# Optimization experiments

Measured on AMD Instinct MI355X. Metric: run time of the kernel, lower is better.

## Reference

```python
import jax, jax.numpy as jnp
import numpy as np

B, N, E, F, C = 4, 10000, 160000, 128, 128
NUM_ITERATIONS = 3  # num_iterations init arg


def setup_inputs() -> dict:
    key = jax.random.key(0)
    ks = jax.random.split(key, 8)
    objects = jax.random.normal(ks[0], (B, N, F), dtype=jnp.float32)
    connections = jax.random.randint(ks[1], (B, E, 2), 0, N, dtype=jnp.int32)
    # small init scales keep exp() in the attention numerically tame (mirrors
    # glorot/orthogonal-scale weights at init)
    object_state_W = jax.random.normal(ks[2], (F, C), dtype=jnp.float32) * (1.0 / np.sqrt(F))
    state_attention_W = jax.random.normal(ks[3], (C, C), dtype=jnp.float32) * 0.05
    linked_state_attention_W = jax.random.normal(ks[4], (C, C), dtype=jnp.float32) * 0.05
    linked_state_W = jax.random.normal(ks[5], (C, C), dtype=jnp.float32) * (1.0 / np.sqrt(C))
    attention_b = jnp.zeros((C,), dtype=jnp.float32)
    state_b = jnp.zeros((C,), dtype=jnp.float32)
    return {
        "objects": objects,
        "object_state_W": object_state_W,
        "state_attention_W": state_attention_W,
        "linked_state_attention_W": linked_state_attention_W,
        "attention_b": attention_b,
        "linked_state_W": linked_state_W,
        "state_b": state_b,
        "connections": connections,
    }


def reference(objects, object_state_W, state_attention_W, linked_state_attention_W,
              attention_b, linked_state_W, state_b, connections):
    # bidirectional: double edges with both orientations  [B, 2E]
    src = jnp.concatenate([connections[:, :, 0], connections[:, :, 1]], axis=1)
    dst = jnp.concatenate([connections[:, :, 1], connections[:, :, 0]], axis=1)

    # initial states: [B, N, C]
    states = jnp.tanh(jnp.einsum('bnf,fc->bnc', objects, object_state_W) + state_b)

    def step_one(states_b, src_b, dst_b):
        # states_b: [N, C]; src_b/dst_b: [2E]
        states_aW = states_b @ state_attention_W          # [N, C]
        linked_aW = states_b @ linked_state_attention_W   # [N, C]
        # per-edge unnormalized attention  [2E, C]
        attention = jnp.exp(states_aW[src_b] + linked_aW[dst_b] + attention_b)
        # scatter-add normalization; self edge contributes 1 (exp(0))
        attention_norm = jnp.ones_like(states_b).at[src_b].add(attention)  # [N, C]
        self_attention = 1.0 / attention_norm
        attention = attention / attention_norm[src_b]
        # weighted neighbor aggregation
        attented = attention * states_b[dst_b]                              # [2E, C]
        linked_gated = jnp.zeros_like(states_b).at[src_b].add(attented)     # [N, C]
        return jnp.tanh(states_b * self_attention + linked_gated @ linked_state_W + state_b)

    step = jax.vmap(step_one)
    for _ in range(NUM_ITERATIONS):
        states = step(states, src, dst)
    return states
```

## Files before the change

### kernel.cpp

```cpp
#include <hip/hip_runtime.h>
#include <hip/hip_bf16.h>


#define BATCH 4
#define NNODE 10000
#define NEDGE 160000
#define TWOE  (2*NEDGE)
#define MROWS (BATCH*NNODE)
#define NCHUNK 64
#define CHUNKE (NEDGE/NCHUNK)
#define PADN  10240
#define EDPAD (TWOE + 8*NNODE)

typedef unsigned short u16;
typedef unsigned int   u32;
typedef __attribute__((ext_vector_type(8))) short bf16x8_t;
typedef __attribute__((ext_vector_type(4))) float f32x4_t;

__device__ __forceinline__ float b2f(u16 h){ return __uint_as_float(((u32)h) << 16); }
__device__ __forceinline__ u16 f2bf(float f){
  u32 u = __float_as_uint(f);
  return (u16)((u + 0x7fffu + ((u >> 16) & 1u)) >> 16);
}
__device__ __forceinline__ float fast_tanh(float x){
  float e = __expf(2.0f * x);
  return fmaf(-2.0f, __builtin_amdgcn_rcpf(e + 1.0f), 1.0f);
}

__device__ __forceinline__ void chunk_of(int blk, int& b, int& c){
  int xcd = blk & 7;
  b = xcd >> 1;
  c = ((blk >> 3) << 1) | (xcd & 1);
}

__global__ void __launch_bounds__(256) k1_prep_hist(const int* __restrict__ conn,
    u16* __restrict__ partial,
    const void* __restrict__ objects,
    const void* __restrict__ Wo, const void* __restrict__ Wa,
    const void* __restrict__ Wla, const void* __restrict__ Wl,
    const void* __restrict__ ab, const void* __restrict__ sb,
    int* __restrict__ flag, u16* __restrict__ Wt, float* __restrict__ biasf){
  __shared__ u32 hist[NNODE / 2];
  __shared__ int zc, hc;
  if (blockIdx.x < 256){
    int b, c; chunk_of(blockIdx.x, b, c);
    for (int n = threadIdx.x; n < NNODE / 2; n += 256) hist[n] = 0;
    __syncthreads();
    const int2* cp = (const int2*)conn + (size_t)b * NEDGE + c * CHUNKE;
    for (int i = threadIdx.x; i < CHUNKE; i += 256){
      int2 e = cp[i];
      atomicAdd(&hist[e.x >> 1], 1u << ((e.x & 1) << 4));
      atomicAdd(&hist[e.y >> 1], 1u << ((e.y & 1) << 4));
    }
    __syncthreads();
    u16* prow = partial + (size_t)(b * NCHUNK + c) * PADN;
    for (int n = threadIdx.x; n < NNODE; n += 256)
      prow[n] = (u16)(hist[n >> 1] >> ((n & 1) << 4));
  } else {
    if (threadIdx.x == 0){ zc = 0; hc = 0; }
    __syncthreads();
    const u32* objw = (const u32*)objects;
    int z = 0, hcnt = 0;
    for (int i = threadIdx.x; i < 1024; i += 256){
      u32 lo = objw[i] & 0xffffu;
      if (lo == 0) z++;
      if (((lo >> 7) & 0xffu) >= 160u) hcnt++;
    }
    atomicAdd(&zc, z); atomicAdd(&hc, hcnt);
    __syncthreads();
    bool f = (hc > 0 || zc > 512);
    int p = blockIdx.x - 256;
    if (p == 0 && threadIdx.x == 0) *flag = f ? 1 : 0;
    int idx = p * 256 + threadIdx.x;
    if (idx < 65536){
      int m = idx >> 14, k = (idx >> 7) & 127, c = idx & 127;
      const void* src = (m == 0) ? Wo : (m == 1) ? Wa : (m == 2) ? Wla : Wl;
      u16 h = f ? f2bf(((const float*)src)[k * 128 + c]) : ((const u16*)src)[k * 128 + c];
      Wt[m * 16384 + c * 128 + k] = h;
    } else {
      int t = idx - 65536;
      const void* src = (t < 128) ? sb : ab;
      int i = t & 127;
      biasf[t] = f ? ((const float*)src)[i] : b2f(((const u16*)src)[i]);
    }
  }
}

__global__ void __launch_bounds__(256) csr_colscan(u16* __restrict__ partial,
    int* __restrict__ row_start, int* __restrict__ bsum, int* __restrict__ deg){
  int b = blockIdx.x / 40, w = blockIdx.x % 40;
  int n = w * 256 + threadIdx.x;
  u32 run = 0;
  if (n < NNODE){
    #pragma unroll 8
    for (int c = 0; c < NCHUNK; c++){
      size_t idx = (size_t)(b * NCHUNK + c) * PADN + n;
      u32 v = partial[idx];
      partial[idx] = (u16)run;
      run += v;
    }
  }
  u32 pad = (run + 7u) & ~7u;
  __shared__ u32 buf[256];
  buf[threadIdx.x] = pad;
  __syncthreads();
  for (int off = 1; off < 256; off <<= 1){
    u32 x = (threadIdx.x >= (unsigned)off) ? buf[threadIdx.x - off] : 0;
    __syncthreads();
    buf[threadIdx.x] += x;
    __syncthreads();
  }
  u32 incl = buf[threadIdx.x];
  if (n < NNODE){
    row_start[b * (NNODE + 1) + n] = (int)(incl - pad);
    deg[b * NNODE + n] = (int)run;
  }
  if (threadIdx.x == 255) bsum[blockIdx.x] = (int)incl;
}

__global__ void scanC(int* __restrict__ row_start, const int* __restrict__ bsum){
  int b = blockIdx.x / 40, j = blockIdx.x % 40;
  int n = j * 256 + threadIdx.x;
  int off = 0;
  for (int q = b * 40; q < b * 40 + j; q++) off += bsum[q];
  if (n < NNODE) row_start[b * (NNODE + 1) + n] += off;
  if (j == 39 && threadIdx.x == 0)
    row_start[b * (NNODE + 1) + NNODE] = off + bsum[b * 40 + 39];
}

__device__ __forceinline__ void gemm_tile4(const u16* __restrict__ arow,
    const u16* __restrict__ wt, int lm, int lq, int cofs, f32x4_t acc[4]){
  #pragma unroll
  for (int ks = 0; ks < 4; ks++){
    bf16x8_t a = *(const bf16x8_t*)(arow + ks * 32);
    #pragma unroll
    for (int nb = 0; nb < 4; nb++){
      bf16x8_t bfr = *(const bf16x8_t*)(wt + (cofs + nb * 16 + lm) * 128 + ks * 32 + lq * 8);
      acc[nb] = __builtin_amdgcn_mfma_f32_16x16x32_bf16(a, bfr, acc[nb], 0, 0, 0);
    }
  }
}

__device__ __forceinline__ void gemm_tile4_packed(const u32* __restrict__ Lrow,
    const u16* __restrict__ wt, int lm, int lq, int cofs, f32x4_t acc[4]){
  #pragma unroll
  for (int ks = 0; ks < 4; ks++){
    uint4 wa = *(const uint4*)(Lrow + ks * 32 + lq * 8);
    uint4 wb = *(const uint4*)(Lrow + ks * 32 + lq * 8 + 4);
    bf16x8_t a;
    a[0] = (short)wa.x; a[1] = (short)wa.y; a[2] = (short)wa.z; a[3] = (short)wa.w;
    a[4] = (short)wb.x; a[5] = (short)wb.y; a[6] = (short)wb.z; a[7] = (short)wb.w;
    #pragma unroll
    for (int nb = 0; nb < 4; nb++){
      bf16x8_t bfr = *(const bf16x8_t*)(wt + (cofs + nb * 16 + lm) * 128 + ks * 32 + lq * 8);
      acc[nb] = __builtin_amdgcn_mfma_f32_16x16x32_bf16(a, bfr, acc[nb], 0, 0, 0);
    }
  }
}

__device__ __forceinline__ void phase2_awlaw4(const u16* __restrict__ ldstile,
    const u16* __restrict__ Wt, const float* __restrict__ biasf,
    int lm, int lq, int cofs, int r0, _Float16* __restrict__ eat,
    u32* __restrict__ ghw){
  const u16* Wta  = Wt + 16384;
  const u16* Wtla = Wt + 32768;
  const u16* ldsrow = ldstile + lm * 136 + lq * 8;
  f32x4_t accA[4], accL[4];
  #pragma unroll
  for (int i = 0; i < 4; i++){ accA[i] = (f32x4_t){0.f,0.f,0.f,0.f}; accL[i] = (f32x4_t){0.f,0.f,0.f,0.f}; }
  #pragma unroll
  for (int ks = 0; ks < 4; ks++){
    bf16x8_t a = *(const bf16x8_t*)(ldsrow + ks * 32);
    #pragma unroll
    for (int nb = 0; nb < 4; nb++){
      bf16x8_t ba = *(const bf16x8_t*)(Wta  + (cofs + nb * 16 + lm) * 128 + ks * 32 + lq * 8);
      bf16x8_t bl = *(const bf16x8_t*)(Wtla + (cofs + nb * 16 + lm) * 128 + ks * 32 + lq * 8);
      accA[nb] = __builtin_amdgcn_mfma_f32_16x16x32_bf16(a, ba, accA[nb], 0, 0, 0);
      accL[nb] = __builtin_amdgcn_mfma_f32_16x16x32_bf16(a, bl, accL[nb], 0, 0, 0);
    }
  }
  #pragma unroll
  for (int nb = 0; nb < 4; nb++){
    int col = cofs + nb * 16 + lm;
    float bb = biasf[128 + col];
    #pragma unroll
    for (int i = 0; i < 4; i++){
      int row = r0 + lq * 4 + i;
      float ea = fminf(__expf(accA[nb][i]), 60000.0f);
      eat[(lq * 4 + i) * 128 + col] = (_Float16)ea;
      _Float16 elh = (_Float16)fminf(__expf(accL[nb][i] + bb), 60000.0f);
      u16 sbf = ldstile[(lq * 4 + i) * 136 + col];
      _Float16 sh = (_Float16)b2f(sbf);
      u32 elu = (u32)(*(const u16*)&elh);
      u32 shu = (u32)(*(const u16*)&sh);
      ghw[(size_t)row * 64 + (col & 63)] = elu | (shu << 16);
    }
  }
}

__device__ __forceinline__ void eah_writeback(const _Float16* __restrict__ eat,
    _Float16* __restrict__ eah, int blk_r0, int tid){
  const uint4* src = (const uint4*)eat;
  uint4* dst = (uint4*)(eah + (size_t)blk_r0 * 128);
  dst[tid]       = src[tid];
  dst[tid + 256] = src[tid + 256];
}

__device__ __forceinline__ void fused_init_body(int blk, int tid,
    const void* __restrict__ obj_raw, const int* __restrict__ flag,
    const u16* __restrict__ Wt, const float* __restrict__ biasf,
    _Float16* __restrict__ eah, u32* __restrict__ gat0, u32* __restrict__ gat1,
    u16* __restrict__ lds, _Float16* __restrict__ eat){
  const int lane = tid & 63, wave = tid >> 6;
  const int t = wave >> 1, ch = wave & 1, cofs = ch * 64;
  const int r0 = blk * 32 + t * 16;
  const int lm = lane & 15, lq = lane >> 4;
  u16* ldsT = lds + t * 2176;
  _Float16* eatT = eat + t * 2048;
  f32x4_t acc[4];
  #pragma unroll
  for (int i = 0; i < 4; i++) acc[i] = (f32x4_t){0.f, 0.f, 0.f, 0.f};
  if (*flag){
    const float* arow = (const float*)obj_raw + (size_t)(r0 + lm) * 128 + lq * 8;
    #pragma unroll
    for (int ks = 0; ks < 4; ks++){
      float4 fa = *(const float4*)(arow + ks * 32);
      float4 fb = *(const float4*)(arow + ks * 32 + 4);
      bf16x8_t a;
      a[0] = (short)f2bf(fa.x); a[1] = (short)f2bf(fa.y);
      a[2] = (short)f2bf(fa.z); a[3] = (short)f2bf(fa.w);
      a[4] = (short)f2bf(fb.x); a[5] = (short)f2bf(fb.y);
      a[6] = (short)f2bf(fb.z); a[7] = (short)f2bf(fb.w);
      #pragma unroll
      for (int nb = 0; nb < 4; nb++){
        bf16x8_t bfr = *(const bf16x8_t*)(Wt + (cofs + nb * 16 + lm) * 128 + ks * 32 + lq * 8);
        acc[nb] = __builtin_amdgcn_mfma_f32_16x16x32_bf16(a, bfr, acc[nb], 0, 0, 0);
      }
    }
  } else {
    gemm_tile4((const u16*)obj_raw + (size_t)(r0 + lm) * 128 + lq * 8, Wt, lm, lq, cofs, acc);
  }
  #pragma unroll
  for (int nb = 0; nb < 4; nb++){
    int col = cofs + nb * 16 + lm;
    float bb = biasf[col];
    #pragma unroll
    for (int i = 0; i < 4; i++)
      ldsT[(lq * 4 + i) * 136 + col] = f2bf(fast_tanh(acc[nb][i] + bb));
  }
  __syncthreads();
  phase2_awlaw4(ldsT, Wt, biasf, lm, lq, cofs, r0, eatT, ch ? gat1 : gat0);
  __syncthreads();
  eah_writeback(eat, eah, blk * 32, tid);
}

__global__ void __launch_bounds__(256) k4_init_fill_pad(
    const void* __restrict__ obj_raw, const int* __restrict__ flag,
    const u16* __restrict__ Wt, const float* __restrict__ biasf,
    _Float16* __restrict__ eah, u32* __restrict__ gat0, u32* __restrict__ gat1,
    const int* __restrict__ conn, const u16* __restrict__ partial,
    const int* __restrict__ row_start, int* __restrict__ edge_dst,
    const int* __restrict__ deg){
  __shared__ __align__(16) char smem[16896];
  int blk = blockIdx.x;
  if (blk < 1250){
    u16* lds = (u16*)smem;
    _Float16* eat = (_Float16*)(smem + 8704);
    fused_init_body(blk, (int)threadIdx.x, obj_raw, flag, Wt, biasf,
                    eah, gat0, gat1, lds, eat);
  } else if (blk < 1506){
    int b, c; chunk_of(blk - 1250, b, c);
    u32* cur = (u32*)smem;
    const u16* prow = partial + (size_t)(b * NCHUNK + c) * PADN;
    const int* rs = row_start + b * (NNODE + 1);
    const int2* cp = (const int2*)conn + (size_t)b * NEDGE + c * CHUNKE;
    int* edb = edge_dst + (size_t)b * EDPAD;
    for (int q = 0; q < 4; q++){
      int n0 = q * 2500;
      for (int n = threadIdx.x; n < 2500; n += 256)
        cur[n] = (u32)rs[n0 + n] + prow[n0 + n];
      __syncthreads();
      for (int i = threadIdx.x; i < CHUNKE; i += 256){
        int2 e = cp[i];
        int rx = e.x - n0, ry = e.y - n0;
        if ((unsigned)rx < 2500u){ u32 p1 = atomicAdd(&cur[rx], 1); edb[p1] = e.y; }
        if ((unsigned)ry < 2500u){ u32 p2 = atomicAdd(&cur[ry], 1); edb[p2] = e.x; }
      }
      __syncthreads();
    }
  } else {
    int p = blk - 1506;
    if (p == 0){
      size_t base = (size_t)MROWS * 64;
      gat0[base + threadIdx.x] = 0;
      gat1[base + threadIdx.x] = 0;
    }
    int b = p / 40, j = p % 40;
    const int* rs = row_start + b * (NNODE + 1);
    int sent = 40000 - 9999 * b;
    int* edb = edge_dst + (size_t)b * EDPAD;
    if (j == 0){
      int T = rs[NNODE];
      for (int q = T + (int)threadIdx.x; q < EDPAD; q += 256) edb[q] = sent;
    }
    int n = j * 256 + threadIdx.x;
    if (n < NNODE){
      int s = rs[n] + deg[b * NNODE + n];
      int epad = rs[n + 1];
      for (int q = s; q < epad; q++) edb[q] = sent;
    }
  }
}

__global__ void __launch_bounds__(256) fused_mid(const u32* __restrict__ lgsa,
    const u16* __restrict__ Wt, const float* __restrict__ biasf,
    _Float16* __restrict__ eah, u32* __restrict__ gat0, u32* __restrict__ gat1){
  __shared__ u16 lds[2][16 * 136];
  __shared__ _Float16 eat[2][16 * 128];
  const int lane = threadIdx.x & 63, wave = threadIdx.x >> 6;
  const int t = wave >> 1, ch = wave & 1, cofs = ch * 64;
  const int r0 = blockIdx.x * 32 + t * 16;
  const int lm = lane & 15, lq = lane >> 4;
  f32x4_t acc[4];
  #pragma unroll
  for (int i = 0; i < 4; i++) acc[i] = (f32x4_t){0.f, 0.f, 0.f, 0.f};
  gemm_tile4_packed(lgsa + (size_t)(r0 + lm) * 128, Wt + 49152, lm, lq, cofs, acc);
  #pragma unroll
  for (int nb = 0; nb < 4; nb++){
    int col = cofs + nb * 16 + lm;
    float bb = biasf[col];
    #pragma unroll
    for (int i = 0; i < 4; i++){
      int row = r0 + lq * 4 + i;
      u32 v = lgsa[(size_t)row * 128 + col];
      u16 hb = (u16)(v >> 16);
      float sa = (float)(*(const _Float16*)&hb);
      lds[t][(lq * 4 + i) * 136 + col] = f2bf(fast_tanh(sa + acc[nb][i] + bb));
    }
  }
  __syncthreads();
  phase2_awlaw4(&lds[t][0], Wt, biasf, lm, lq, cofs, r0, &eat[t][0], ch ? gat1 : gat0);
  __syncthreads();
  eah_writeback(&eat[0][0], eah, blockIdx.x * 32, threadIdx.x);
}

__global__ void __launch_bounds__(256) final_out(const u32* __restrict__ lgsa,
    const u16* __restrict__ Wt, const float* __restrict__ biasf,
    const int* __restrict__ flag, void* __restrict__ outp){
  const int lane = threadIdx.x & 63, wave = threadIdx.x >> 6;
  const int t = wave >> 1, ch = wave & 1, cofs = ch * 64;
  const int r0 = blockIdx.x * 32 + t * 16;
  const int lm = lane & 15, lq = lane >> 4;
  bool f32out = (*flag != 0);
  f32x4_t acc[4];
  #pragma unroll
  for (int i = 0; i < 4; i++) acc[i] = (f32x4_t){0.f, 0.f, 0.f, 0.f};
  gemm_tile4_packed(lgsa + (size_t)(r0 + lm) * 128, Wt + 49152, lm, lq, cofs, acc);
  #pragma unroll
  for (int nb = 0; nb < 4; nb++){
    int col = cofs + nb * 16 + lm;
    float bb = biasf[col];
    #pragma unroll
    for (int i = 0; i < 4; i++){
      int row = r0 + lq * 4 + i;
      u32 vv = lgsa[(size_t)row * 128 + col];
      u16 hb = (u16)(vv >> 16);
      float sa = (float)(*(const _Float16*)&hb);
      float v = fast_tanh(sa + acc[nb][i] + bb);
      if (f32out) ((float*)outp)[(size_t)row * 128 + col] = v;
      else        ((u16*)  outp)[(size_t)row * 128 + col] = f2bf(v);
    }
  }
}

__device__ __forceinline__ void acc_mix(u32 g, float one, float& a1, float& a2){
  asm("v_fma_mix_f32 %0, %2, %3, %0 op_sel:[0,0,0] op_sel_hi:[1,0,0]\n\t"
      "v_fma_mix_f32 %1, %2, %2, %1 op_sel:[0,1,0] op_sel_hi:[1,1,0]"
      : "+v"(a1), "+v"(a2)
      : "v"(g), "v"(one));
}

__device__ __forceinline__ u32 gath1(const u32* __restrict__ gh, int d, int c){
  const u32* p = (const u32*)((const char*)gh + ((size_t)(u32)d << 8));
  return p[c];
}

#define LDIDX(d, p) { const int* ep_ = (p); _Pragma("unroll") \
  for (int j = 0; j < 8; j++) d[j] = __builtin_amdgcn_readfirstlane(ep_[j]); }
#define GATH8(g, d) { _Pragma("unroll") \
  for (int j = 0; j < 8; j++) g[j] = gath1(gh, d[j], c); }
#define CONS8(g, s1, s2, t1, t2) { _Pragma("unroll") \
  for (int j = 0; j < 8; j++) acc_mix(g[j], one, (j & 1) ? t1 : s1, (j & 1) ? t2 : s2); }

__global__ void __launch_bounds__(128, 6) edge_kernel(const _Float16* __restrict__ eah,
    const u32* __restrict__ gat0, const u32* __restrict__ gat1,
    const int* __restrict__ row_start, const int* __restrict__ edge_dst,
    u32* __restrict__ lgsa){
  int blk = blockIdx.x;
  int xcd = blk & 7;
  int b = xcd >> 1, h = xcd & 1;
  int i = blk >> 3;
  int w = (int)(threadIdx.x >> 6);
  int nA = i * 4 + w * 2, nB = nA + 1;
  int c = threadIdx.x & 63;
  const u32* gh = (h ? gat1 : gat0) + (size_t)b * NNODE * 64;
  const int* rs = row_start + b * (NNODE + 1);
  int eA  = __builtin_amdgcn_readfirstlane(rs[nA]);
  int eA1 = __builtin_amdgcn_readfirstlane(rs[nA + 1]);
  int eB1 = __builtin_amdgcn_readfirstlane(rs[nB + 1]);
  int eB = eA1;
  const int* ed = edge_dst + (size_t)b * EDPAD;

  float eaA = (float)eah[(size_t)(b * NNODE + nA) * 128 + h * 64 + c];
  float eaB = (float)eah[(size_t)(b * NNODE + nB) * 128 + h * 64 + c];
  u32 selfA = gh[((size_t)nA << 6) + c];
  u32 selfB = gh[((size_t)nB << 6) + c];
  const float one = 1.0f;

  float sA1=0.f, sA2=0.f, tA1=0.f, tA2=0.f;
  float sB1=0.f, sB2=0.f, tB1=0.f, tB2=0.f;
  int ngA = (eA1 - eA) >> 3, ngB = (eB1 - eB) >> 3;
  int dA[8], dB[8]; u32 gA[8], gB[8], hA[8], hB[8];

  if (ngA){ LDIDX(dA, ed + eA); }
  if (ngB){ LDIDX(dB, ed + eB); }
  if (ngA){ GATH8(gA, dA); eA += 8; LDIDX(dA, ed + eA); }
  if (ngB){ GATH8(gB, dB); eB += 8; LDIDX(dB, ed + eB); }

  int m = ngA < ngB ? ngA : ngB;
  int cons = 0;
  for (; cons + 2 <= m; cons += 2){
    GATH8(hA, dA); eA += 8; LDIDX(dA, ed + eA);
    GATH8(hB, dB); eB += 8; LDIDX(dB, ed + eB);
    CONS8(gA, sA1, sA2, tA1, tA2);
    CONS8(gB, sB1, sB2, tB1, tB2);
    GATH8(gA, dA); eA += 8; LDIDX(dA, ed + eA);
    GATH8(gB, dB); eB += 8; LDIDX(dB, ed + eB);
    CONS8(hA, sA1, sA2, tA1, tA2);
    CONS8(hB, sB1, sB2, tB1, tB2);
  }

  { int rem = ngA - cons;
    if (rem > 0){
      int k = 1;
      for (; k + 1 < rem; k += 2){
        GATH8(hA, dA); eA += 8; LDIDX(dA, ed + eA);
        CONS8(gA, sA1, sA2, tA1, tA2);
        GATH8(gA, dA); eA += 8; LDIDX(dA, ed + eA);
        CONS8(hA, sA1, sA2, tA1, tA2);
      }
      if (k < rem){
        GATH8(hA, dA);
        CONS8(gA, sA1, sA2, tA1, tA2);
        CONS8(hA, sA1, sA2, tA1, tA2);
      } else {
        CONS8(gA, sA1, sA2, tA1, tA2);
      }
    }
  }
  { int rem = ngB - cons;
    if (rem > 0){
      int k = 1;
      for (; k + 1 < rem; k += 2){
        GATH8(hB, dB); eB += 8; LDIDX(dB, ed + eB);
        CONS8(gB, sB1, sB2, tB1, tB2);
        GATH8(gB, dB); eB += 8; LDIDX(dB, ed + eB);
        CONS8(hB, sB1, sB2, tB1, tB2);
      }
      if (k < rem){
        GATH8(hB, dB);
        CONS8(gB, sB1, sB2, tB1, tB2);
        CONS8(hB, sB1, sB2, tB1, tB2);
      } else {
        CONS8(gB, sB1, sB2, tB1, tB2);
      }
    }
  }

  sA1 += tA1; sA2 += tA2; sB1 += tB1; sB2 += tB2;
  { float inv = __builtin_amdgcn_rcpf(fmaf(eaA, sA1, 1.0f));
    float lg = eaA * sA2 * inv;
    u16 hb = (u16)(selfA >> 16);
    float s_self = (float)(*(const _Float16*)&hb);
    _Float16 hs = (_Float16)(s_self * inv);
    u32 pk = (u32)f2bf(lg) | ((u32)(*(const u16*)&hs) << 16);
    lgsa[(size_t)(b * NNODE + nA) * 128 + h * 64 + c] = pk; }
  { float inv = __builtin_amdgcn_rcpf(fmaf(eaB, sB1, 1.0f));
    float lg = eaB * sB2 * inv;
    u16 hb = (u16)(selfB >> 16);
    float s_self = (float)(*(const _Float16*)&hb);
    _Float16 hs = (_Float16)(s_self * inv);
    u32 pk = (u32)f2bf(lg) | ((u32)(*(const u16*)&hs) << 16);
    lgsa[(size_t)(b * NNODE + nB) * 128 + h * 64 + c] = pk; }
}

extern "C" void kernel_launch(void* const* d_in, const int* in_sizes, int n_in,
                              void* d_out, int out_size, void* d_ws, size_t ws_size,
                              hipStream_t stream){
  (void)in_sizes; (void)n_in; (void)ws_size; (void)out_size;
  const void* objects = d_in[0];
  const void* Wo      = d_in[1];
  const void* Wa      = d_in[2];
  const void* Wla     = d_in[3];
  const void* attn_b  = d_in[4];
  const void* Wl      = d_in[5];
  const void* state_b = d_in[6];
  const int*  conn    = (const int*)d_in[7];

  char* base = (char*)d_ws;
  size_t off = 0;
  auto alloc = [&](size_t bytes) -> char* {
    char* p = base + off;
    off = (off + bytes + 255) & ~(size_t)255;
    return p;
  };
  int*      flag      = (int*)     alloc(256);
  u16*      Wt        = (u16*)     alloc((size_t)4 * 16384 * 2);
  float*    biasf     = (float*)   alloc(256 * 4);
  _Float16* eah       = (_Float16*)alloc((size_t)MROWS * 128 * 2);
  u32*      gat0      = (u32*)     alloc((size_t)(MROWS + 4) * 64 * 4);
  u32*      gat1      = (u32*)     alloc((size_t)(MROWS + 4) * 64 * 4);
  u32*      lgsa      = (u32*)     alloc((size_t)MROWS * 128 * 4);
  u16*      partial   = (u16*)     alloc((size_t)BATCH * NCHUNK * PADN * 2);
  int*      row_start = (int*)     alloc((size_t)BATCH * (NNODE + 1) * 4);
  int*      edge_dst  = (int*)     alloc((size_t)BATCH * EDPAD * 4);
  int*      deg       = (int*)     alloc((size_t)MROWS * 4);
  int*      bsum      = (int*)     alloc(160 * 4);

  k1_prep_hist<<<513, 256, 0, stream>>>(conn, partial, objects, Wo, Wa, Wla, Wl,
                                        attn_b, state_b, flag, Wt, biasf);
  csr_colscan<<<160, 256, 0, stream>>>(partial, row_start, bsum, deg);
  scanC<<<160, 256, 0, stream>>>(row_start, bsum);
  k4_init_fill_pad<<<1666, 256, 0, stream>>>(objects, flag, Wt, biasf, eah,
                                             gat0, gat1, conn, partial,
                                             row_start, edge_dst, deg);

  edge_kernel<<<MROWS / 2, 128, 0, stream>>>(eah, gat0, gat1, row_start, edge_dst, lgsa);
  fused_mid<<<MROWS / 32, 256, 0, stream>>>(lgsa, Wt, biasf, eah, gat0, gat1);
  edge_kernel<<<MROWS / 2, 128, 0, stream>>>(eah, gat0, gat1, row_start, edge_dst, lgsa);
  fused_mid<<<MROWS / 32, 256, 0, stream>>>(lgsa, Wt, biasf, eah, gat0, gat1);
  edge_kernel<<<MROWS / 2, 128, 0, stream>>>(eah, gat0, gat1, row_start, edge_dst, lgsa);
  final_out<<<MROWS / 32, 256, 0, stream>>>(lgsa, Wt, biasf, flag, d_out);
}
```

Before: 352.3 us.

## Replace chunked LDS CSR fill with global atomic cursors per node

The CSR fill no longer uses per-chunk prefix offsets held in LDS across four node-range passes. Each block now takes a 1000-edge segment and claims slots with global atomicAdd on a per-node cursor array that scanC initializes from row_start. The colscan no longer writes exclusive chunk offsets back to partial. This removes the four passes over the connection chunk and the LDS staging, at the cost of contended global atomics and a nondeterministic edge order within each row, which changes floating-point summation order.

```diff
diff --git a/kernel.cpp b/kernel.cpp
--- a/kernel.cpp
+++ b/kernel.cpp
@@ -95,9 +95,7 @@
     #pragma unroll 8
     for (int c = 0; c < NCHUNK; c++){
       size_t idx = (size_t)(b * NCHUNK + c) * PADN + n;
-      u32 v = partial[idx];
-      partial[idx] = (u16)run;
-      run += v;
+      run += partial[idx];
     }
   }
   u32 pad = (run + 7u) & ~7u;
@@ -118,12 +116,17 @@
   if (threadIdx.x == 255) bsum[blockIdx.x] = (int)incl;
 }
 
-__global__ void scanC(int* __restrict__ row_start, const int* __restrict__ bsum){
+__global__ void scanC(int* __restrict__ row_start, const int* __restrict__ bsum,
+                      int* __restrict__ cur_g){
   int b = blockIdx.x / 40, j = blockIdx.x % 40;
   int n = j * 256 + threadIdx.x;
   int off = 0;
   for (int q = b * 40; q < b * 40 + j; q++) off += bsum[q];
-  if (n < NNODE) row_start[b * (NNODE + 1) + n] += off;
+  if (n < NNODE){
+    int v = row_start[b * (NNODE + 1) + n] + off;
+    row_start[b * (NNODE + 1) + n] = v;
+    cur_g[b * NNODE + n] = v;
+  }
   if (j == 39 && threadIdx.x == 0)
     row_start[b * (NNODE + 1) + NNODE] = off + bsum[b * 40 + 39];
 }
@@ -258,9 +261,9 @@
     const void* __restrict__ obj_raw, const int* __restrict__ flag,
     const u16* __restrict__ Wt, const float* __restrict__ biasf,
     _Float16* __restrict__ eah, u32* __restrict__ gat0, u32* __restrict__ gat1,
-    const int* __restrict__ conn, const u16* __restrict__ partial,
-    const int* __restrict__ row_start, int* __restrict__ edge_dst,
-    const int* __restrict__ deg){
+    const int* __restrict__ conn, const int* __restrict__ row_start,
+    int* __restrict__ edge_dst, const int* __restrict__ deg,
+    int* __restrict__ cur_g){
   __shared__ __align__(16) char smem[16896];
   int blk = blockIdx.x;
   if (blk < 1250){
@@ -268,28 +271,19 @@
     _Float16* eat = (_Float16*)(smem + 8704);
     fused_init_body(blk, (int)threadIdx.x, obj_raw, flag, Wt, biasf,
                     eah, gat0, gat1, lds, eat);
-  } else if (blk < 1506){
-    int b, c; chunk_of(blk - 1250, b, c);
-    u32* cur = (u32*)smem;
-    const u16* prow = partial + (size_t)(b * NCHUNK + c) * PADN;
-    const int* rs = row_start + b * (NNODE + 1);
-    const int2* cp = (const int2*)conn + (size_t)b * NEDGE + c * CHUNKE;
+  } else if (blk < 1890){
+    int p = blk - 1250;
+    int b = p / 160, seg = p % 160;
+    const int2* cp = (const int2*)conn + (size_t)b * NEDGE + seg * 1000;
     int* edb = edge_dst + (size_t)b * EDPAD;
-    for (int q = 0; q < 4; q++){
-      int n0 = q * 2500;
-      for (int n = threadIdx.x; n < 2500; n += 256)
-        cur[n] = (u32)rs[n0 + n] + prow[n0 + n];
-      __syncthreads();
-      for (int i = threadIdx.x; i < CHUNKE; i += 256){
-        int2 e = cp[i];
-        int rx = e.x - n0, ry = e.y - n0;
-        if ((unsigned)rx < 2500u){ u32 p1 = atomicAdd(&cur[rx], 1); edb[p1] = e.y; }
-        if ((unsigned)ry < 2500u){ u32 p2 = atomicAdd(&cur[ry], 1); edb[p2] = e.x; }
-      }
-      __syncthreads();
+    int* cg = cur_g + b * NNODE;
+    for (int i = threadIdx.x; i < 1000; i += 256){
+      int2 e = cp[i];
+      int p1 = atomicAdd(&cg[e.x], 1); edb[p1] = e.y;
+      int p2 = atomicAdd(&cg[e.y], 1); edb[p2] = e.x;
     }
   } else {
-    int p = blk - 1506;
+    int p = blk - 1890;
     if (p == 0){
       size_t base = (size_t)MROWS * 64;
       gat0[base + threadIdx.x] = 0;
@@ -525,15 +519,16 @@
   int*      row_start = (int*)     alloc((size_t)BATCH * (NNODE + 1) * 4);
   int*      edge_dst  = (int*)     alloc((size_t)BATCH * EDPAD * 4);
   int*      deg       = (int*)     alloc((size_t)MROWS * 4);
+  int*      cur_g     = (int*)     alloc((size_t)MROWS * 4);
   int*      bsum      = (int*)     alloc(160 * 4);
 
   k1_prep_hist<<<513, 256, 0, stream>>>(conn, partial, objects, Wo, Wa, Wla, Wl,
                                         attn_b, state_b, flag, Wt, biasf);
   csr_colscan<<<160, 256, 0, stream>>>(partial, row_start, bsum, deg);
-  scanC<<<160, 256, 0, stream>>>(row_start, bsum);
-  k4_init_fill_pad<<<1666, 256, 0, stream>>>(objects, flag, Wt, biasf, eah,
-                                             gat0, gat1, conn, partial,
-                                             row_start, edge_dst, deg);
+  scanC<<<160, 256, 0, stream>>>(row_start, bsum, cur_g);
+  k4_init_fill_pad<<<2050, 256, 0, stream>>>(objects, flag, Wt, biasf, eah,
+                                             gat0, gat1, conn, row_start,
+                                             edge_dst, deg, cur_g);
 
   edge_kernel<<<MROWS / 2, 128, 0, stream>>>(eah, gat0, gat1, row_start, edge_dst, lgsa);
   fused_mid<<<MROWS / 32, 256, 0, stream>>>(lgsa, Wt, biasf, eah, gat0, gat1);
```

Measured after the change: 409.7 us. 16.3% more time.
